# Optimization experiments

Measured on AMD Instinct MI355X. Metric: run time of the kernel, lower is better.

The kernel has to match this reference:

```python
import jax, jax.numpy as jnp
import numpy as np

DT = 1e-3   # time step (s)
DX = 10.0   # grid spacing (m)


def laplacian(u):
    # 5-point stencil with zero-Dirichlet boundaries; u: (B, ny, nx)
    up = jnp.pad(u, ((0, 0), (1, 1), (1, 1)))
    return (up[:, 2:, 1:-1] + up[:, :-2, 1:-1]
            + up[:, 1:-1, 2:] + up[:, 1:-1, :-2]
            - 4.0 * u) / (DX * DX)


def setup_inputs() -> dict:
    key = jax.random.key(0)
    ks = jax.random.split(key, 6)
    B, ny, nx, nt, R = 4, 256, 256, 300, 128
    x = jax.random.normal(ks[0], (B, nt), dtype=jnp.float32)          # source wavelets
    vp = 1500.0 + 1000.0 * jax.random.uniform(ks[1], (ny, nx), dtype=jnp.float32)
    src_y = jax.random.randint(ks[2], (B,), 2, ny - 2)
    src_x = jax.random.randint(ks[3], (B,), 2, nx - 2)
    rec_y = jax.random.randint(ks[4], (R,), 2, ny - 2)
    rec_x = jax.random.randint(ks[5], (R,), 2, nx - 2)
    return {"x": x, "vp": vp, "src_y": src_y, "src_x": src_x,
            "rec_y": rec_y, "rec_x": rec_x}


def reference(x, vp, src_y, src_x, rec_y, rec_x):
    # x: (B, nt) source amplitudes; vp: (ny, nx) velocity model.
    B = x.shape[0]
    ny, nx = vp.shape
    c2dt2 = (vp * vp) * (DT * DT)        # (ny, nx), vp^2 dt^2
    bidx = jnp.arange(B)

    def step(carry, xt):
        h1, h2 = carry                                    # u_t, u_{t-1}
        hn = 2.0 * h1 - h2 + c2dt2[None] * laplacian(h1)  # leapfrog update
        hn = hn.at[bidx, src_y, src_x].add(xt)            # source injection (scatter)
        rec = hn[:, rec_y, rec_x]                         # probe gather -> (B, R)
        return (hn, h1), rec

    h0 = jnp.zeros((B, ny, nx), dtype=x.dtype)
    _, recs = jax.lax.scan(step, (h0, h0), x.T)           # recs: (nt, B, R)
    y = jnp.transpose(recs, (0, 2, 1))                    # (nt, R, B) as in torch permute(1,2,0)
    return y
```

## Files before the change

### kernel.cpp

```cpp
#include <hip/hip_runtime.h>


constexpr int B_   = 4;
constexpr int NY   = 256;
constexpr int NX   = 256;
constexpr int NT   = 300;
constexpr int RCV  = 128;

constexpr int QB   = 16;
constexpr int RB   = NY / QB;
constexpr int W    = 8;
constexpr int EXT  = RB + 2 * W;
constexpr int NBLK = B_ * QB;
constexpr int NTHR = 512;
constexpr int ROWS = 4;
constexpr int NW   = EXT / ROWS;
constexpr int SLABR = EXT + 2;
constexpr int PUBR = 2 * W - 1;
constexpr int LINKS = B_ * (QB - 1);
constexpr size_t HALO_FLOATS = (size_t)LINKS * 2 * 2 * PUBR * NX;

__device__ __forceinline__ void at_store2(float* p, float a, float b) {
    float2 v = make_float2(a, b);
    unsigned long long u;
    __builtin_memcpy(&u, &v, 8);
    __hip_atomic_store((unsigned long long*)p, u, __ATOMIC_RELAXED,
                       __HIP_MEMORY_SCOPE_AGENT);
}
__device__ __forceinline__ float2 at_load2(const float* p) {
    unsigned long long u = __hip_atomic_load((const unsigned long long*)p,
                                             __ATOMIC_RELAXED,
                                             __HIP_MEMORY_SCOPE_AGENT);
    float2 v;
    __builtin_memcpy(&v, &u, 8);
    return v;
}

__global__ __launch_bounds__(NTHR, 1)
void wave_tb2(const float* __restrict__ x,
              const float* __restrict__ vp,
              const int*   __restrict__ src_y,
              const int*   __restrict__ src_x,
              const int*   __restrict__ rec_y,
              const int*   __restrict__ rec_x,
              float*       __restrict__ y,
              float*       __restrict__ halo,
              int*         __restrict__ flags)
{
    __shared__ float slabs[2][SLABR][NX];

    const int tid = threadIdx.x, blk = blockIdx.x;
    const int b = blk >> 4, q = blk & 15;
    const int r0 = q * RB;
    const int w = tid >> 6, lane = tid & 63;
    const int c0 = lane * 4;
    const int e0 = ROWS * w;

    for (int i = tid; i < 2 * SLABR * NX; i += NTHR) ((float*)slabs)[i] = 0.f;

    const float scale = 1e-8f;
    float hA[ROWS][4], hB[ROWS][4], c2[ROWS][4];
#pragma unroll
    for (int rr = 0; rr < ROWS; ++rr) {
        const int gr = r0 - W + e0 + rr;
        if (gr >= 0 && gr < NY) {
            float4 v = *reinterpret_cast<const float4*>(&vp[gr * NX + c0]);
            c2[rr][0] = v.x * v.x * scale; c2[rr][1] = v.y * v.y * scale;
            c2[rr][2] = v.z * v.z * scale; c2[rr][3] = v.w * v.w * scale;
        } else {
#pragma unroll
            for (int j = 0; j < 4; ++j) c2[rr][j] = 0.f;
        }
#pragma unroll
        for (int j = 0; j < 4; ++j) { hA[rr][j] = 0.f; hB[rr][j] = 0.f; }
    }

    const int sy = src_y[b], sx = src_x[b];
    const int es = sy - r0 + W;
    const bool src_mine = (es >= e0) && (es < e0 + ROWS) && ((sx >> 2) == lane);
    const int s_j = sx & 3;

    bool rec_mine = false; int rec_addr = 0; float* yp = nullptr;
    if (tid < RCV) {
        const int ry = rec_y[tid], rx = rec_x[tid];
        rec_mine = (ry >= r0) && (ry < r0 + RB);
        rec_addr = (ry - r0 + W + 1) * NX + rx;
        yp = y + tid * B_ + b;
    }

    const float* xb = x + b * NT;
    int* upflag = flags + blk - 1;
    int* dnflag = flags + blk + 1;

    __syncthreads();
    int exch = 0;

#define STEP(HO, HN, tt)                                                       \
    {                                                                          \
        const int cur = (tt) & 1, nxt = ((tt) + 1) & 1;                        \
        if ((tt) > 0 && rec_mine)        \
            yp[(size_t)((tt) - 1) * RCV * B_] =                                \
                ((const float*)slabs[cur])[rec_addr];                          \
        const float4 u4 = *reinterpret_cast<const float4*>(&slabs[cur][e0][c0]);\
        const float4 d4 = *reinterpret_cast<const float4*>(&slabs[cur][e0+ROWS+1][c0]);\
        const float ua[4] = {u4.x, u4.y, u4.z, u4.w};                          \
        const float da[4] = {d4.x, d4.y, d4.z, d4.w};                          \
        const float xt = xb[tt];                                               \
        _Pragma("unroll")                                                      \
        for (int rr = 0; rr < ROWS; ++rr) {                                    \
            float lv = __shfl_up(HO[rr][3], 1);   if (lane == 0)  lv = 0.f;    \
            float rv = __shfl_down(HO[rr][0], 1); if (lane == 63) rv = 0.f;    \
            _Pragma("unroll")                                                  \
            for (int j = 0; j < 4; ++j) {                                      \
                const float uu = (rr == 0)      ? ua[j] : HO[rr-1][j];         \
                const float dd = (rr == ROWS-1) ? da[j] : HO[rr+1][j];         \
                const float ll = (j == 0) ? lv : HO[rr][j-1];                  \
                const float rr2= (j == 3) ? rv : HO[rr][j+1];                  \
                HN[rr][j] = 2.f*HO[rr][j] - HN[rr][j]                          \
                          + c2[rr][j]*(uu + dd + ll + rr2 - 4.f*HO[rr][j]);    \
            }                                                                  \
        }                                                                      \
        if (src_mine) {                                                        \
            _Pragma("unroll")                                                  \
            for (int rr = 0; rr < ROWS; ++rr)                                  \
                _Pragma("unroll")                                              \
                for (int j = 0; j < 4; ++j)                                    \
                    if (e0 + rr == es && j == s_j) HN[rr][j] += xt;            \
        }                                                                      \
        _Pragma("unroll")                                                      \
        for (int rr = 0; rr < ROWS; ++rr)                                      \
            *reinterpret_cast<float4*>(&slabs[nxt][e0+1+rr][c0]) =             \
                make_float4(HN[rr][0], HN[rr][1], HN[rr][2], HN[rr][3]);       \
        if ((((tt) + 1) & 7) == 0) {                                           \
            ++exch;                                                            \
            const int slot = exch & 1;                                         \
            if (q < QB-1 && w >= 4 && w <= 5) {      \
                float* p = halo + (((size_t)(b*(QB-1)+q)*2 + 0)*2 + slot)*PUBR*NX;\
                _Pragma("unroll")                                              \
                for (int rr = 0; rr < ROWS; ++rr) {                            \
                    const int ext = e0 + rr;                                   \
                    at_store2(&p[(ext-16)*NX + c0],     HN[rr][0], HN[rr][1]); \
                    at_store2(&p[(ext-16)*NX + c0 + 2], HN[rr][2], HN[rr][3]); \
                    if (ext >= 17) {                                           \
                        at_store2(&p[(8+ext-17)*NX + c0],     HO[rr][0], HO[rr][1]);\
                        at_store2(&p[(8+ext-17)*NX + c0 + 2], HO[rr][2], HO[rr][3]);\
                    }                                                          \
                }                                                              \
            }                                                                  \
            if (q > 0 && w >= 2 && w <= 3) {           \
                float* p = halo + (((size_t)(b*(QB-1)+q-1)*2 + 1)*2 + slot)*PUBR*NX;\
                _Pragma("unroll")                                              \
                for (int rr = 0; rr < ROWS; ++rr) {                            \
                    const int ext = e0 + rr;                                   \
                    at_store2(&p[(ext-8)*NX + c0],     HN[rr][0], HN[rr][1]);  \
                    at_store2(&p[(ext-8)*NX + c0 + 2], HN[rr][2], HN[rr][3]);  \
                    if (ext < 15) {                                            \
                        at_store2(&p[(8+ext-8)*NX + c0],     HO[rr][0], HO[rr][1]);\
                        at_store2(&p[(8+ext-8)*NX + c0 + 2], HO[rr][2], HO[rr][3]);\
                    }                                                          \
                }                                                              \
            }                                                                  \
            __syncthreads();    \
            if (tid == 0)                                                      \
                __hip_atomic_store(&flags[blk], exch, __ATOMIC_RELAXED,        \
                                   __HIP_MEMORY_SCOPE_AGENT);                  \
            if (q > 0 && w <= 1) {                   \
                while (__hip_atomic_load(upflag, __ATOMIC_RELAXED,             \
                        __HIP_MEMORY_SCOPE_AGENT) < exch)                      \
                    __builtin_amdgcn_s_sleep(1);                               \
                const float* p = halo + (((size_t)(b*(QB-1)+q-1)*2 + 0)*2 + slot)*PUBR*NX;\
                _Pragma("unroll")                                              \
                for (int rr = 0; rr < ROWS; ++rr) {                            \
                    const int ext = e0 + rr;                                   \
                    float2 a0 = at_load2(&p[ext*NX + c0]);                     \
                    float2 a1 = at_load2(&p[ext*NX + c0 + 2]);                 \
                    HN[rr][0]=a0.x; HN[rr][1]=a0.y; HN[rr][2]=a1.x; HN[rr][3]=a1.y;\
                    *reinterpret_cast<float4*>(&slabs[nxt][ext+1][c0]) =       \
                        make_float4(a0.x, a0.y, a1.x, a1.y);                   \
                    if (ext >= 1) {                                            \
                        float2 b0 = at_load2(&p[(8+ext-1)*NX + c0]);           \
                        float2 b1 = at_load2(&p[(8+ext-1)*NX + c0 + 2]);       \
                        HO[rr][0]=b0.x; HO[rr][1]=b0.y; HO[rr][2]=b1.x; HO[rr][3]=b1.y;\
                    }                                                          \
                }                                                              \
            }                                                                  \
            if (q < QB-1 && w >= NW-2) {             \
                while (__hip_atomic_load(dnflag, __ATOMIC_RELAXED,             \
                        __HIP_MEMORY_SCOPE_AGENT) < exch)                      \
                    __builtin_amdgcn_s_sleep(1);                               \
                const float* p = halo + (((size_t)(b*(QB-1)+q)*2 + 1)*2 + slot)*PUBR*NX;\
                _Pragma("unroll")                                              \
                for (int rr = 0; rr < ROWS; ++rr) {                            \
                    const int ext = e0 + rr;                                   \
                    float2 a0 = at_load2(&p[(ext-24)*NX + c0]);                \
                    float2 a1 = at_load2(&p[(ext-24)*NX + c0 + 2]);            \
                    HN[rr][0]=a0.x; HN[rr][1]=a0.y; HN[rr][2]=a1.x; HN[rr][3]=a1.y;\
                    *reinterpret_cast<float4*>(&slabs[nxt][ext+1][c0]) =       \
                        make_float4(a0.x, a0.y, a1.x, a1.y);                   \
                    if (ext < 31) {                                            \
                        float2 b0 = at_load2(&p[(8+ext-24)*NX + c0]);          \
                        float2 b1 = at_load2(&p[(8+ext-24)*NX + c0 + 2]);      \
                        HO[rr][0]=b0.x; HO[rr][1]=b0.y; HO[rr][2]=b1.x; HO[rr][3]=b1.y;\
                    }                                                          \
                }                                                              \
            }                                                                  \
            __syncthreads();              \
        } else {                                                               \
            __syncthreads();                        \
        }                                                                      \
    }

    for (int t = 0; t < NT; t += 2) {
        STEP(hA, hB, t)
        STEP(hB, hA, t + 1)
    }
#undef STEP

    if (rec_mine)
        yp[(size_t)(NT - 1) * RCV * B_] = ((const float*)slabs[0])[rec_addr];
}

extern "C" void kernel_launch(void* const* d_in, const int* in_sizes, int n_in,
                              void* d_out, int out_size, void* d_ws, size_t ws_size,
                              hipStream_t stream) {
    const float* x     = (const float*)d_in[0];
    const float* vp    = (const float*)d_in[1];
    const int*   src_y = (const int*)d_in[2];
    const int*   src_x = (const int*)d_in[3];
    const int*   rec_y = (const int*)d_in[4];
    const int*   rec_x = (const int*)d_in[5];
    float*       y     = (float*)d_out;

    float* halo  = (float*)d_ws;
    int*   flags = (int*)((char*)d_ws + HALO_FLOATS * sizeof(float));

    hipMemsetAsync(d_ws, 0, HALO_FLOATS * sizeof(float) + NBLK * sizeof(int),
                   stream);

    wave_tb2<<<NBLK, NTHR, 0, stream>>>(x, vp, src_y, src_x, rec_y, rec_x,
                                        y, halo, flags);
}
```

Measured before the change: 365.8 us.

## Remap blocks for XCD locality and use dual-path flag polling for halo exchange

The grid grows to 128 blocks, with b = blk&7, so that neighbouring q-slabs of the same shot land on the same XCD under round-robin dispatch. Half of the blocks exit at once. Halo publishing switches from 64-bit atomic stores to plain float4 stores. A separate fast flag, padded to its own line, is written with a volatile store and read with sc0 loads, meant to take the XCD-local L2 path, while a fenced agent-scope flag is kept as the fallback. The aim is lower latency for the inter-block halo exchange. It relies on an undocumented assumption about how blocks map to XCDs and on cache-coherence behaviour, and it adds a guard timeout that could silently read stale data.

```diff
diff --git a/kernel.cpp b/kernel.cpp
--- a/kernel.cpp
+++ b/kernel.cpp
@@ -11,22 +11,20 @@
 constexpr int RB   = NY / QB;
 constexpr int W    = 8;
 constexpr int EXT  = RB + 2 * W;
-constexpr int NBLK = B_ * QB;
+constexpr int GRIDB= 128;
 constexpr int NTHR = 512;
 constexpr int ROWS = 4;
 constexpr int NW   = EXT / ROWS;
-constexpr int SLABR = EXT + 2;
+constexpr int SLABR= EXT + 2;
 constexpr int PUBR = 2 * W - 1;
-constexpr int LINKS = B_ * (QB - 1);
+constexpr int LINKS= B_ * (QB - 1);
 constexpr size_t HALO_FLOATS = (size_t)LINKS * 2 * 2 * PUBR * NX;
-
-__device__ __forceinline__ void at_store2(float* p, float a, float b) {
-    float2 v = make_float2(a, b);
-    unsigned long long u;
-    __builtin_memcpy(&u, &v, 8);
-    __hip_atomic_store((unsigned long long*)p, u, __ATOMIC_RELAXED,
-                       __HIP_MEMORY_SCOPE_AGENT);
-}
+constexpr size_t HALO_BYTES  = HALO_FLOATS * sizeof(float);
+constexpr int FSTR = 64;
+constexpr size_t CTRL_INTS = (size_t)GRIDB * FSTR + GRIDB;
+
+typedef float f32x4 __attribute__((ext_vector_type(4)));
+
 __device__ __forceinline__ float2 at_load2(const float* p) {
     unsigned long long u = __hip_atomic_load((const unsigned long long*)p,
                                              __ATOMIC_RELAXED,
@@ -35,26 +33,68 @@
     __builtin_memcpy(&v, &u, 8);
     return v;
 }
+__device__ __forceinline__ int load_sc0_i32(const int* p) {
+    int v;
+    asm volatile("global_load_dword %0, %1, off sc0\n\ts_waitcnt vmcnt(0)"
+                 : "=v"(v) : "v"(p) : "memory");
+    return v;
+}
+__device__ __forceinline__ void pub_row(float* p, int row, int c0,
+                                        const float v[4]) {
+    *reinterpret_cast<float4*>(p + row * NX + c0) =
+        make_float4(v[0], v[1], v[2], v[3]);
+}
+__device__ __forceinline__ void ing_row(const float* p, int row, int c0,
+                                        float v[4], bool fast) {
+    const float* src = p + row * NX + c0;
+    if (fast) {
+        f32x4 t;
+        asm volatile("global_load_dwordx4 %0, %1, off sc0\n\ts_waitcnt vmcnt(0)"
+                     : "=v"(t) : "v"(src) : "memory");
+        v[0] = t.x; v[1] = t.y; v[2] = t.z; v[3] = t.w;
+    } else {
+        float2 a = at_load2(src), b2 = at_load2(src + 2);
+        v[0] = a.x; v[1] = a.y; v[2] = b2.x; v[3] = b2.y;
+    }
+}
+__device__ __forceinline__ bool dual_wait(const int* fastp, const int* slowp,
+                                          int target) {
+    int guard = 0;
+    for (;;) {
+        if (load_sc0_i32(fastp) >= target) return true;
+        if (__hip_atomic_load(slowp, __ATOMIC_RELAXED,
+                              __HIP_MEMORY_SCOPE_AGENT) >= target) return false;
+        if (++guard > (1 << 22)) return false;
+        __builtin_amdgcn_s_sleep(1);
+    }
+}
 
 __global__ __launch_bounds__(NTHR, 1)
-void wave_tb2(const float* __restrict__ x,
-              const float* __restrict__ vp,
-              const int*   __restrict__ src_y,
-              const int*   __restrict__ src_x,
-              const int*   __restrict__ rec_y,
-              const int*   __restrict__ rec_x,
-              float*       __restrict__ y,
-              float*       __restrict__ halo,
-              int*         __restrict__ flags)
+void wave_dual(const float* __restrict__ x,
+               const float* __restrict__ vp,
+               const int*   __restrict__ src_y,
+               const int*   __restrict__ src_x,
+               const int*   __restrict__ rec_y,
+               const int*   __restrict__ rec_x,
+               float*       __restrict__ y,
+               float*       __restrict__ halo,
+               int*         __restrict__ ctrl)
 {
+    const int blk = blockIdx.x;
+    const int b = blk & 7;
+    if (b >= B_) return;
+    const int q = blk >> 3;
+
     __shared__ float slabs[2][SLABR][NX];
 
-    const int tid = threadIdx.x, blk = blockIdx.x;
-    const int b = blk >> 4, q = blk & 15;
+    const int tid = threadIdx.x;
     const int r0 = q * RB;
     const int w = tid >> 6, lane = tid & 63;
     const int c0 = lane * 4;
     const int e0 = ROWS * w;
+
+    int* fastf = ctrl;
+    int* slowf = ctrl + GRIDB * FSTR;
 
     for (int i = tid; i < 2 * SLABR * NX; i += NTHR) ((float*)slabs)[i] = 0.f;
 
@@ -89,8 +129,6 @@
     }
 
     const float* xb = x + b * NT;
-    int* upflag = flags + blk - 1;
-    int* dnflag = flags + blk + 1;
 
     __syncthreads();
     int exch = 0;
@@ -98,7 +136,7 @@
 #define STEP(HO, HN, tt)                                                       \
     {                                                                          \
         const int cur = (tt) & 1, nxt = ((tt) + 1) & 1;                        \
-        if ((tt) > 0 && rec_mine)        \
+        if ((tt) > 0 && rec_mine)                                              \
             yp[(size_t)((tt) - 1) * RCV * B_] =                                \
                 ((const float*)slabs[cur])[rec_addr];                          \
         const float4 u4 = *reinterpret_cast<const float4*>(&slabs[cur][e0][c0]);\
@@ -133,80 +171,66 @@
                 make_float4(HN[rr][0], HN[rr][1], HN[rr][2], HN[rr][3]);       \
         if ((((tt) + 1) & 7) == 0) {                                           \
             ++exch;                                                            \
-            const int slot = exch & 1;                                         \
+            const size_t soff = (size_t)(exch & 1) * PUBR * NX;                \
             if (q < QB-1 && w >= 4 && w <= 5) {      \
-                float* p = halo + (((size_t)(b*(QB-1)+q)*2 + 0)*2 + slot)*PUBR*NX;\
-                _Pragma("unroll")                                              \
-                for (int rr = 0; rr < ROWS; ++rr) {                            \
-                    const int ext = e0 + rr;                                   \
-                    at_store2(&p[(ext-16)*NX + c0],     HN[rr][0], HN[rr][1]); \
-                    at_store2(&p[(ext-16)*NX + c0 + 2], HN[rr][2], HN[rr][3]); \
-                    if (ext >= 17) {                                           \
-                        at_store2(&p[(8+ext-17)*NX + c0],     HO[rr][0], HO[rr][1]);\
-                        at_store2(&p[(8+ext-17)*NX + c0 + 2], HO[rr][2], HO[rr][3]);\
+                float* p = halo + (((size_t)(b*(QB-1)+q)*2 + 0)*2 * PUBR)*NX + soff;\
+                _Pragma("unroll")                                              \
+                for (int rr = 0; rr < ROWS; ++rr) {                            \
+                    const int ext = e0 + rr;                                   \
+                    pub_row(p, ext - 16, c0, HN[rr]);                          \
+                    if (ext >= 17) pub_row(p, 8 + ext - 17, c0, HO[rr]);       \
+                }                                                              \
+            }                                                                  \
+            if (q > 0 && w >= 2 && w <= 3) {           \
+                float* p = halo + (((size_t)(b*(QB-1)+q-1)*2 + 1)*2 * PUBR)*NX + soff;\
+                _Pragma("unroll")                                              \
+                for (int rr = 0; rr < ROWS; ++rr) {                            \
+                    const int ext = e0 + rr;                                   \
+                    pub_row(p, ext - 8, c0, HN[rr]);                           \
+                    if (ext < 15) pub_row(p, 8 + ext - 8, c0, HO[rr]);         \
+                }                                                              \
+            }                                                                  \
+            __syncthreads();                 \
+            if (tid == 0) {                                                    \
+                ((volatile int*)fastf)[blk * FSTR] = exch;  \
+                __threadfence();                    \
+                __hip_atomic_store(&slowf[blk], exch, __ATOMIC_RELAXED,        \
+                                   __HIP_MEMORY_SCOPE_AGENT);                  \
+            }                                                                  \
+            if (q > 0 && w <= 1) {                   \
+                const bool fast = dual_wait(&fastf[(blk-8)*FSTR],              \
+                                            &slowf[blk-8], exch);              \
+                const float* p = halo + (((size_t)(b*(QB-1)+q-1)*2 + 0)*2 * PUBR)*NX + soff;\
+                _Pragma("unroll")                                              \
+                for (int rr = 0; rr < ROWS; ++rr) {                            \
+                    const int ext = e0 + rr;                                   \
+                    if (ext < 8) {                                             \
+                        ing_row(p, ext, c0, HN[rr], fast);                     \
+                        *reinterpret_cast<float4*>(&slabs[nxt][ext+1][c0]) =   \
+                            make_float4(HN[rr][0],HN[rr][1],HN[rr][2],HN[rr][3]);\
+                        if (ext >= 1) ing_row(p, 7 + ext, c0, HO[rr], fast);   \
                     }                                                          \
                 }                                                              \
             }                                                                  \
-            if (q > 0 && w >= 2 && w <= 3) {           \
-                float* p = halo + (((size_t)(b*(QB-1)+q-1)*2 + 1)*2 + slot)*PUBR*NX;\
-                _Pragma("unroll")                                              \
-                for (int rr = 0; rr < ROWS; ++rr) {                            \
-                    const int ext = e0 + rr;                                   \
-                    at_store2(&p[(ext-8)*NX + c0],     HN[rr][0], HN[rr][1]);  \
-                    at_store2(&p[(ext-8)*NX + c0 + 2], HN[rr][2], HN[rr][3]);  \
-                    if (ext < 15) {                                            \
-                        at_store2(&p[(8+ext-8)*NX + c0],     HO[rr][0], HO[rr][1]);\
-                        at_store2(&p[(8+ext-8)*NX + c0 + 2], HO[rr][2], HO[rr][3]);\
+            if (q < QB-1 && w >= NW-2) {             \
+                const bool fast = dual_wait(&fastf[(blk+8)*FSTR],              \
+                                            &slowf[blk+8], exch);              \
+                const float* p = halo + (((size_t)(b*(QB-1)+q)*2 + 1)*2 * PUBR)*NX + soff;\
+                _Pragma("unroll")                                              \
+                for (int rr = 0; rr < ROWS; ++rr) {                            \
+                    const int ext = e0 + rr;                                   \
+                    if (ext >= EXT-8) {                                        \
+                        ing_row(p, ext - (EXT-8), c0, HN[rr], fast);           \
+                        *reinterpret_cast<float4*>(&slabs[nxt][ext+1][c0]) =   \
+                            make_float4(HN[rr][0],HN[rr][1],HN[rr][2],HN[rr][3]);\
+                        if (ext < EXT-1)                                       \
+                            ing_row(p, 8 + ext - (EXT-8), c0, HO[rr], fast);   \
                     }                                                          \
                 }                                                              \
             }                                                                  \
-            __syncthreads();    \
-            if (tid == 0)                                                      \
-                __hip_atomic_store(&flags[blk], exch, __ATOMIC_RELAXED,        \
-                                   __HIP_MEMORY_SCOPE_AGENT);                  \
-            if (q > 0 && w <= 1) {                   \
-                while (__hip_atomic_load(upflag, __ATOMIC_RELAXED,             \
-                        __HIP_MEMORY_SCOPE_AGENT) < exch)                      \
-                    __builtin_amdgcn_s_sleep(1);                               \
-                const float* p = halo + (((size_t)(b*(QB-1)+q-1)*2 + 0)*2 + slot)*PUBR*NX;\
-                _Pragma("unroll")                                              \
-                for (int rr = 0; rr < ROWS; ++rr) {                            \
-                    const int ext = e0 + rr;                                   \
-                    float2 a0 = at_load2(&p[ext*NX + c0]);                     \
-                    float2 a1 = at_load2(&p[ext*NX + c0 + 2]);                 \
-                    HN[rr][0]=a0.x; HN[rr][1]=a0.y; HN[rr][2]=a1.x; HN[rr][3]=a1.y;\
-                    *reinterpret_cast<float4*>(&slabs[nxt][ext+1][c0]) =       \
-                        make_float4(a0.x, a0.y, a1.x, a1.y);                   \
-                    if (ext >= 1) {                                            \
-                        float2 b0 = at_load2(&p[(8+ext-1)*NX + c0]);           \
-                        float2 b1 = at_load2(&p[(8+ext-1)*NX + c0 + 2]);       \
-                        HO[rr][0]=b0.x; HO[rr][1]=b0.y; HO[rr][2]=b1.x; HO[rr][3]=b1.y;\
-                    }                                                          \
-                }                                                              \
-            }                                                                  \
-            if (q < QB-1 && w >= NW-2) {             \
-                while (__hip_atomic_load(dnflag, __ATOMIC_RELAXED,             \
-                        __HIP_MEMORY_SCOPE_AGENT) < exch)                      \
-                    __builtin_amdgcn_s_sleep(1);                               \
-                const float* p = halo + (((size_t)(b*(QB-1)+q)*2 + 1)*2 + slot)*PUBR*NX;\
-                _Pragma("unroll")                                              \
-                for (int rr = 0; rr < ROWS; ++rr) {                            \
-                    const int ext = e0 + rr;                                   \
-                    float2 a0 = at_load2(&p[(ext-24)*NX + c0]);                \
-                    float2 a1 = at_load2(&p[(ext-24)*NX + c0 + 2]);            \
-                    HN[rr][0]=a0.x; HN[rr][1]=a0.y; HN[rr][2]=a1.x; HN[rr][3]=a1.y;\
-                    *reinterpret_cast<float4*>(&slabs[nxt][ext+1][c0]) =       \
-                        make_float4(a0.x, a0.y, a1.x, a1.y);                   \
-                    if (ext < 31) {                                            \
-                        float2 b0 = at_load2(&p[(8+ext-24)*NX + c0]);          \
-                        float2 b1 = at_load2(&p[(8+ext-24)*NX + c0 + 2]);      \
-                        HO[rr][0]=b0.x; HO[rr][1]=b0.y; HO[rr][2]=b1.x; HO[rr][3]=b1.y;\
-                    }                                                          \
-                }                                                              \
-            }                                                                  \
-            __syncthreads();              \
+            __syncthreads();                                                   \
         } else {                                                               \
-            __syncthreads();                        \
+            __syncthreads();                                                   \
         }                                                                      \
     }
 
@@ -231,12 +255,11 @@
     const int*   rec_x = (const int*)d_in[5];
     float*       y     = (float*)d_out;
 
-    float* halo  = (float*)d_ws;
-    int*   flags = (int*)((char*)d_ws + HALO_FLOATS * sizeof(float));
-
-    hipMemsetAsync(d_ws, 0, HALO_FLOATS * sizeof(float) + NBLK * sizeof(int),
-                   stream);
-
-    wave_tb2<<<NBLK, NTHR, 0, stream>>>(x, vp, src_y, src_x, rec_y, rec_x,
-                                        y, halo, flags);
-}
+    float* halo = (float*)d_ws;
+    int*   ctrl = (int*)((char*)d_ws + HALO_BYTES);
+
+    hipMemsetAsync(d_ws, 0, HALO_BYTES + CTRL_INTS * sizeof(int), stream);
+
+    wave_dual<<<GRIDB, NTHR, 0, stream>>>(x, vp, src_y, src_x, rec_y, rec_x,
+                                          y, halo, ctrl);
+}
```

Result: slower. 393.9 us (+7.7%).
